# Kernel tuning notes

Hardware: AMD Instinct MI355X
Metric: run time of the kernel (lower is better)

## Reference

```python
import jax, jax.numpy as jnp
import numpy as np

B, S, H, L = 8, 4096, 768, 256   # batch, seq_len, hidden_size, num_lines (= line_ids.max()+1)
ATT_HID = 1024                    # attention MLP hidden dim from nn.Linear(hidden,1024)


def setup_inputs() -> dict:
    key = jax.random.key(0)
    k0, k1, k2, k3 = jax.random.split(key, 4)
    token_hidden = jax.random.normal(k0, (B, S, H), dtype=jnp.float32)
    line_ids = jax.random.randint(k1, (B, S), 0, L)  # all valid; -1 would mark invalid
    W1 = jax.random.normal(k2, (H, ATT_HID), dtype=jnp.float32) * 0.02
    b1 = jnp.zeros((ATT_HID,), jnp.float32)
    W2 = jax.random.normal(k3, (ATT_HID, 1), dtype=jnp.float32) * 0.02
    b2 = jnp.zeros((1,), jnp.float32)
    return {"token_hidden": token_hidden, "line_ids": line_ids,
            "W1": W1, "b1": b1, "W2": W2, "b2": b2}


def reference(token_hidden, line_ids, W1, b1, W2, b2):
    b, s, h = token_hidden.shape
    num_lines = L
    n_seg = b * num_lines + 1  # last segment is a dump slot for invalid (-1) tokens

    # attention scores: Linear -> tanh -> Linear, squeeze(-1)  [b, s]
    scores = (jnp.tanh(token_hidden @ W1 + b1) @ W2 + b2)[..., 0]

    valid = (line_ids >= 0).reshape(-1)                                   # [b*s]
    seg = jnp.where(line_ids >= 0,
                    jnp.arange(b)[:, None] * num_lines + line_ids,
                    b * num_lines).reshape(-1)                            # [b*s]
    s_flat = jnp.where(valid, scores.reshape(-1), -jnp.inf)

    # segment-wise stable softmax
    m = jax.ops.segment_max(s_flat, seg, num_segments=n_seg)
    m = jnp.where(jnp.isfinite(m), m, 0.0)  # empty segments -> safe 0
    e = jnp.where(valid, jnp.exp(scores.reshape(-1) - m[seg]), 0.0)
    denom = jax.ops.segment_sum(e, seg, num_segments=n_seg)
    w = e / jnp.maximum(denom[seg], 1e-20)                                # [b*s]

    # weighted sum of tokens per (batch, line) segment
    feats = jax.ops.segment_sum(token_hidden.reshape(-1, h) * w[:, None],
                                seg, num_segments=n_seg)
    line_features = feats[: b * num_lines].reshape(b, num_lines, h)

    counts = jax.ops.segment_sum(valid.astype(jnp.float32), seg, num_segments=n_seg)
    line_mask = counts[: b * num_lines].reshape(b, num_lines) > 0
    return line_features, line_mask
```

## Files before the change

kernel.cpp:

```cpp
#include <hip/hip_runtime.h>
#include <hip/hip_bf16.h>
#include <string.h>

#define M_TOK 32768
#define H_DIM 768
#define AH    1024
#define NSEG  2048
#define CAP   96
#define CONV_BLOCKS 12288

typedef __attribute__((ext_vector_type(8))) __bf16 bf16x8;
typedef __attribute__((ext_vector_type(4))) float f32x4;

__device__ __forceinline__ float tanh_fast(float x) {
  float e = __expf(2.0f * x);
  return 1.0f - 2.0f * __builtin_amdgcn_rcpf(e + 1.0f);
}

__device__ __forceinline__ float bf2f(unsigned short u) {
  unsigned int v = (unsigned int)u << 16;
  float f;
  memcpy(&f, &v, 4);
  return f;
}

__global__ __launch_bounds__(256) void prep_kernel(
    const float* __restrict__ W1, __hip_bfloat16* __restrict__ W1t,
    const int* __restrict__ line_ids, int* __restrict__ cursor,
    int* __restrict__ order, const float4* __restrict__ X4,
    uint4* __restrict__ Xb4) {
  __shared__ float tile[32][33];
  if (blockIdx.x < 768) {
    int nt = blockIdx.x & 31, ktile = blockIdx.x >> 5;
    int n0 = nt * 32, k0 = ktile * 32;
    int tx = threadIdx.x & 31, ty = threadIdx.x >> 5;
    for (int r = ty; r < 32; r += 8)
      tile[r][tx] = W1[(size_t)(k0 + r) * AH + n0 + tx];
    __syncthreads();
    for (int r = ty; r < 32; r += 8)
      W1t[(size_t)(n0 + r) * H_DIM + k0 + tx] = __float2bfloat16(tile[tx][r]);
  } else if (blockIdx.x < 896) {
    int t = (blockIdx.x - 768) * 256 + threadIdx.x;
    int lid = line_ids[t];
    if (lid >= 0) {
      int seg = (t >> 12) * 256 + lid;
      int pos = atomicAdd(&cursor[seg], 1);
      if (pos < CAP) order[seg * CAP + pos] = t;
    }
  } else {
    int i = (blockIdx.x - 896) * 256 + threadIdx.x;
    float4 v0 = X4[i * 2];
    float4 v1 = X4[i * 2 + 1];
    __hip_bfloat16 h[8] = {
        __float2bfloat16(v0.x), __float2bfloat16(v0.y),
        __float2bfloat16(v0.z), __float2bfloat16(v0.w),
        __float2bfloat16(v1.x), __float2bfloat16(v1.y),
        __float2bfloat16(v1.z), __float2bfloat16(v1.w)};
    uint4 p;
    memcpy(&p, h, 16);
    Xb4[i] = p;
  }
}

__global__ __launch_bounds__(256) void attn_score_kernel(
    const __hip_bfloat16* __restrict__ Xbg,
    const __hip_bfloat16* __restrict__ W1tg, const float* __restrict__ b1g,
    const float* __restrict__ W2g, float* __restrict__ scores) {
  __shared__ __align__(16) __bf16 As[128 * 64];
  __shared__ __align__(16) __bf16 Bs[128 * 64];

  const int tid = threadIdx.x;
  const int bid = blockIdx.x;
  const int xcd = bid & 7;
  const int s   = bid >> 3;
  const int m0  = (xcd * 32 + (s >> 3)) * 128;
  const int n0  = (s & 7) * 128;
  const int lane = tid & 63;
  const int wave = tid >> 6;
  const int wm   = (wave >> 1) * 64;
  const int wn   = (wave & 1) * 64;
  const int ml   = lane & 15;
  const int gsw  = lane & 7;

  const __bf16* Xb = (const __bf16*)Xbg;
  const __bf16* W  = (const __bf16*)W1tg;

  const int srow = tid >> 3;
  const int scol = ((tid & 7) ^ (srow & 7)) * 8;

  f32x4 acc[4][4];
#pragma unroll
  for (int i = 0; i < 4; i++)
#pragma unroll
    for (int j = 0; j < 4; j++) acc[i][j] = (f32x4)0.f;

  for (int kt = 0; kt < H_DIM; kt += 64) {
#pragma unroll
    for (int p = 0; p < 4; ++p) {
      const __bf16* ga = Xb + (size_t)(m0 + p * 32 + srow) * H_DIM + kt + scol;
      __builtin_amdgcn_global_load_lds(
          (const __attribute__((address_space(1))) void*)ga,
          (__attribute__((address_space(3))) void*)&As[p * 2048 + tid * 8],
          16, 0, 0);
      const __bf16* gb = W + (size_t)(n0 + p * 32 + srow) * H_DIM + kt + scol;
      __builtin_amdgcn_global_load_lds(
          (const __attribute__((address_space(1))) void*)gb,
          (__attribute__((address_space(3))) void*)&Bs[p * 2048 + tid * 8],
          16, 0, 0);
    }
    __syncthreads();

#pragma unroll
    for (int c = 0; c < 2; ++c) {
      const int gq = c * 4 + (lane >> 4);
      const int gp = (gq ^ gsw) * 8;
      bf16x8 af[4], bf[4];
#pragma unroll
      for (int i = 0; i < 4; i++)
        af[i] = *(const bf16x8*)&As[(wm + i * 16 + ml) * 64 + gp];
#pragma unroll
      for (int j = 0; j < 4; j++)
        bf[j] = *(const bf16x8*)&Bs[(wn + j * 16 + ml) * 64 + gp];

#pragma unroll
      for (int i = 0; i < 4; i++)
#pragma unroll
        for (int j = 0; j < 4; j++)
          acc[i][j] = __builtin_amdgcn_mfma_f32_16x16x32_bf16(af[i], bf[j],
                                                              acc[i][j], 0, 0, 0);
    }
    __syncthreads();
  }

  float b1v[4], w2v[4];
#pragma unroll
  for (int j = 0; j < 4; j++) {
    int n = n0 + wn + j * 16 + ml;
    b1v[j] = b1g[n];
    w2v[j] = W2g[n];
  }
  const int q4 = (lane >> 4) * 4;
#pragma unroll
  for (int i = 0; i < 4; i++) {
#pragma unroll
    for (int p = 0; p < 4; p++) {
      float t = 0.f;
#pragma unroll
      for (int j = 0; j < 4; j++)
        t += tanh_fast(acc[i][j][p] + b1v[j]) * w2v[j];
      t += __shfl_xor(t, 1);
      t += __shfl_xor(t, 2);
      t += __shfl_xor(t, 4);
      t += __shfl_xor(t, 8);
      if (ml == 0) atomicAdd(&scores[m0 + wm + i * 16 + q4 + p], t);
    }
  }
}

__global__ __launch_bounds__(256) void aggregate_kernel(
    const ushort* __restrict__ Xb, const float* __restrict__ scores,
    const int* __restrict__ cursor, const int* __restrict__ order,
    float4* __restrict__ out4, float* __restrict__ out_mask) {
  __shared__ float sw[CAP];
  __shared__ int   sidx[CAP];
  __shared__ float wred[4];
  const int seg = blockIdx.x;
  const int tid = threadIdx.x;
  int cnt = cursor[seg];
  if (cnt > CAP) cnt = CAP;
  if (tid == 0) out_mask[seg] = cnt > 0 ? 1.f : 0.f;
  if (cnt == 0) {
    if (tid < H_DIM / 4)
      out4[(size_t)seg * (H_DIM / 4) + tid] = make_float4(0.f, 0.f, 0.f, 0.f);
    return;
  }
  const int lane = tid & 63, wave = tid >> 6;
  float lmax = -3.4e38f;
  if (tid < cnt) {
    int idx = order[seg * CAP + tid];
    sidx[tid] = idx;
    float sc = scores[idx];
    sw[tid] = sc;
    lmax = sc;
  }
#pragma unroll
  for (int d = 1; d < 64; d <<= 1) lmax = fmaxf(lmax, __shfl_xor(lmax, d));
  if (lane == 0) wred[wave] = lmax;
  __syncthreads();
  float m = fmaxf(fmaxf(wred[0], wred[1]), fmaxf(wred[2], wred[3]));
  float lsum = 0.f;
  if (tid < cnt) {
    float e = __expf(sw[tid] - m);
    sw[tid] = e;
    lsum = e;
  }
#pragma unroll
  for (int d = 1; d < 64; d <<= 1) lsum += __shfl_xor(lsum, d);
  __syncthreads();
  if (lane == 0) wred[wave] = lsum;
  __syncthreads();
  float denom = wred[0] + wred[1] + wred[2] + wred[3];
  float inv = __builtin_amdgcn_rcpf(fmaxf(denom, 1e-20f));
  if (tid < cnt) sw[tid] *= inv;
  __syncthreads();
  if (tid < H_DIM / 4) {
    const ushort4* base = (const ushort4*)Xb + tid;
    float4 acc = make_float4(0.f, 0.f, 0.f, 0.f);
    int t = 0;
    for (; t + 4 <= cnt; t += 4) {
      ushort4 u0 = base[(size_t)sidx[t]     * (H_DIM / 4)];
      ushort4 u1 = base[(size_t)sidx[t + 1] * (H_DIM / 4)];
      ushort4 u2 = base[(size_t)sidx[t + 2] * (H_DIM / 4)];
      ushort4 u3 = base[(size_t)sidx[t + 3] * (H_DIM / 4)];
      float w0 = sw[t], w1 = sw[t + 1], w2 = sw[t + 2], w3 = sw[t + 3];
      acc.x += w0 * bf2f(u0.x) + w1 * bf2f(u1.x) + w2 * bf2f(u2.x) + w3 * bf2f(u3.x);
      acc.y += w0 * bf2f(u0.y) + w1 * bf2f(u1.y) + w2 * bf2f(u2.y) + w3 * bf2f(u3.y);
      acc.z += w0 * bf2f(u0.z) + w1 * bf2f(u1.z) + w2 * bf2f(u2.z) + w3 * bf2f(u3.z);
      acc.w += w0 * bf2f(u0.w) + w1 * bf2f(u1.w) + w2 * bf2f(u2.w) + w3 * bf2f(u3.w);
    }
    for (; t < cnt; ++t) {
      ushort4 u = base[(size_t)sidx[t] * (H_DIM / 4)];
      float w = sw[t];
      acc.x += w * bf2f(u.x); acc.y += w * bf2f(u.y);
      acc.z += w * bf2f(u.z); acc.w += w * bf2f(u.w);
    }
    out4[(size_t)seg * (H_DIM / 4) + tid] = acc;
  }
}

extern "C" void kernel_launch(void* const* d_in, const int* in_sizes, int n_in,
                              void* d_out, int out_size, void* d_ws, size_t ws_size,
                              hipStream_t stream) {
  const float* X        = (const float*)d_in[0];
  const int*   line_ids = (const int*)d_in[1];
  const float* W1       = (const float*)d_in[2];
  const float* b1       = (const float*)d_in[3];
  const float* W2       = (const float*)d_in[4];

  char* p = (char*)d_ws;
  __hip_bfloat16* Xb  = (__hip_bfloat16*)p;  p += (size_t)M_TOK * H_DIM * 2;
  __hip_bfloat16* W1t = (__hip_bfloat16*)p;  p += 1572864;
  float* scores  = (float*)p;                p += 131072;
  int*   cursor  = (int*)p;                  p += 8192;
  int*   order   = (int*)p;                  p += (size_t)NSEG * CAP * 4;

  float* out_feats = (float*)d_out;
  float* out_mask  = out_feats + (size_t)NSEG * H_DIM;

  hipMemsetAsync(scores, 0, 131072 + 8192, stream);

  prep_kernel<<<896 + CONV_BLOCKS, 256, 0, stream>>>(
      W1, W1t, line_ids, cursor, order, (const float4*)X, (uint4*)Xb);
  attn_score_kernel<<<2048, 256, 0, stream>>>(Xb, W1t, b1, W2, scores);
  aggregate_kernel<<<NSEG, 256, 0, stream>>>((const ushort*)Xb, scores, cursor,
                                             order, (float4*)out_feats, out_mask);
}
```

Baseline: 252.2 us.

## Replace atomics with deterministic partial scores and in-block segment gathering

```diff
diff --git a/kernel.cpp b/kernel.cpp
--- a/kernel.cpp
+++ b/kernel.cpp
@@ -6,7 +6,7 @@
 #define H_DIM 768
 #define AH    1024
 #define NSEG  2048
-#define CAP   96
+#define LCAP  192
 #define CONV_BLOCKS 12288
 
 typedef __attribute__((ext_vector_type(8))) __bf16 bf16x8;
@@ -26,9 +26,7 @@
 
 __global__ __launch_bounds__(256) void prep_kernel(
     const float* __restrict__ W1, __hip_bfloat16* __restrict__ W1t,
-    const int* __restrict__ line_ids, int* __restrict__ cursor,
-    int* __restrict__ order, const float4* __restrict__ X4,
-    uint4* __restrict__ Xb4) {
+    const float4* __restrict__ X4, uint4* __restrict__ Xb4) {
   __shared__ float tile[32][33];
   if (blockIdx.x < 768) {
     int nt = blockIdx.x & 31, ktile = blockIdx.x >> 5;
@@ -39,16 +37,8 @@
     __syncthreads();
     for (int r = ty; r < 32; r += 8)
       W1t[(size_t)(n0 + r) * H_DIM + k0 + tx] = __float2bfloat16(tile[tx][r]);
-  } else if (blockIdx.x < 896) {
-    int t = (blockIdx.x - 768) * 256 + threadIdx.x;
-    int lid = line_ids[t];
-    if (lid >= 0) {
-      int seg = (t >> 12) * 256 + lid;
-      int pos = atomicAdd(&cursor[seg], 1);
-      if (pos < CAP) order[seg * CAP + pos] = t;
-    }
   } else {
-    int i = (blockIdx.x - 896) * 256 + threadIdx.x;
+    int i = (blockIdx.x - 768) * 256 + threadIdx.x;
     float4 v0 = X4[i * 2];
     float4 v1 = X4[i * 2 + 1];
     __hip_bfloat16 h[8] = {
@@ -65,7 +55,7 @@
 __global__ __launch_bounds__(256) void attn_score_kernel(
     const __hip_bfloat16* __restrict__ Xbg,
     const __hip_bfloat16* __restrict__ W1tg, const float* __restrict__ b1g,
-    const float* __restrict__ W2g, float* __restrict__ scores) {
+    const float* __restrict__ W2g, float* __restrict__ scores2) {
   __shared__ __align__(16) __bf16 As[128 * 64];
   __shared__ __align__(16) __bf16 Bs[128 * 64];
 
@@ -74,7 +64,8 @@
   const int xcd = bid & 7;
   const int s   = bid >> 3;
   const int m0  = (xcd * 32 + (s >> 3)) * 128;
-  const int n0  = (s & 7) * 128;
+  const int nt  = s & 7;
+  const int n0  = nt * 128;
   const int lane = tid & 63;
   const int wave = tid >> 6;
   const int wm   = (wave >> 1) * 64;
@@ -140,6 +131,7 @@
     w2v[j] = W2g[n];
   }
   const int q4 = (lane >> 4) * 4;
+  float tval[4][4];
 #pragma unroll
   for (int i = 0; i < 4; i++) {
 #pragma unroll
@@ -152,34 +144,74 @@
       t += __shfl_xor(t, 2);
       t += __shfl_xor(t, 4);
       t += __shfl_xor(t, 8);
-      if (ml == 0) atomicAdd(&scores[m0 + wm + i * 16 + q4 + p], t);
-    }
+      tval[i][p] = t;
+    }
+  }
+  float* redbuf = (float*)As;
+  if ((wave & 1) && ml == 0) {
+#pragma unroll
+    for (int i = 0; i < 4; i++)
+#pragma unroll
+      for (int p = 0; p < 4; p++)
+        redbuf[wm + i * 16 + q4 + p] = tval[i][p];
+  }
+  __syncthreads();
+  if (!(wave & 1) && ml == 0) {
+#pragma unroll
+    for (int i = 0; i < 4; i++)
+#pragma unroll
+      for (int p = 0; p < 4; p++) {
+        int row = wm + i * 16 + q4 + p;
+        scores2[(size_t)(m0 + row) * 8 + nt] = tval[i][p] + redbuf[row];
+      }
   }
 }
 
 __global__ __launch_bounds__(256) void aggregate_kernel(
-    const ushort* __restrict__ Xb, const float* __restrict__ scores,
-    const int* __restrict__ cursor, const int* __restrict__ order,
-    float4* __restrict__ out4, float* __restrict__ out_mask) {
-  __shared__ float sw[CAP];
-  __shared__ int   sidx[CAP];
+    const ushort* __restrict__ Xb, const float* __restrict__ scores2,
+    const int* __restrict__ line_ids, float4* __restrict__ out4,
+    float* __restrict__ out_mask) {
+  __shared__ int   slist[LCAP];
+  __shared__ float sw[LCAP];
+  __shared__ int   wvc[4];
   __shared__ float wred[4];
   const int seg = blockIdx.x;
-  const int tid = threadIdx.x;
-  int cnt = cursor[seg];
-  if (cnt > CAP) cnt = CAP;
+  const int b = seg >> 8, lid = seg & 255;
+  const int tid = threadIdx.x, lane = tid & 63, wave = tid >> 6;
+  const int base = b * 4096;
+
+  int ids[16];
+#pragma unroll
+  for (int c = 0; c < 16; ++c) ids[c] = line_ids[base + c * 256 + tid];
+
+  int total = 0;
+#pragma unroll
+  for (int c = 0; c < 16; ++c) {
+    bool match = (ids[c] == lid);
+    unsigned long long mask = __ballot(match);
+    if (lane == 0) wvc[wave] = __popcll(mask);
+    __syncthreads();
+    int off = total;
+    for (int w = 0; w < wave; ++w) off += wvc[w];
+    if (match) {
+      int pos = off + __popcll(mask & ((1ull << lane) - 1ull));
+      if (pos < LCAP) slist[pos] = base + c * 256 + tid;
+    }
+    total += wvc[0] + wvc[1] + wvc[2] + wvc[3];
+    __syncthreads();
+  }
+  int cnt = total > LCAP ? LCAP : total;
   if (tid == 0) out_mask[seg] = cnt > 0 ? 1.f : 0.f;
   if (cnt == 0) {
     if (tid < H_DIM / 4)
       out4[(size_t)seg * (H_DIM / 4) + tid] = make_float4(0.f, 0.f, 0.f, 0.f);
     return;
   }
-  const int lane = tid & 63, wave = tid >> 6;
   float lmax = -3.4e38f;
   if (tid < cnt) {
-    int idx = order[seg * CAP + tid];
-    sidx[tid] = idx;
-    float sc = scores[idx];
+    const float4* sp = (const float4*)(scores2 + (size_t)slist[tid] * 8);
+    float4 a = sp[0], c4 = sp[1];
+    float sc = ((a.x + a.y) + (a.z + a.w)) + ((c4.x + c4.y) + (c4.z + c4.w));
     sw[tid] = sc;
     lmax = sc;
   }
@@ -204,14 +236,14 @@
   if (tid < cnt) sw[tid] *= inv;
   __syncthreads();
   if (tid < H_DIM / 4) {
-    const ushort4* base = (const ushort4*)Xb + tid;
+    const ushort4* xb = (const ushort4*)Xb + tid;
     float4 acc = make_float4(0.f, 0.f, 0.f, 0.f);
     int t = 0;
     for (; t + 4 <= cnt; t += 4) {
-      ushort4 u0 = base[(size_t)sidx[t]     * (H_DIM / 4)];
-      ushort4 u1 = base[(size_t)sidx[t + 1] * (H_DIM / 4)];
-      ushort4 u2 = base[(size_t)sidx[t + 2] * (H_DIM / 4)];
-      ushort4 u3 = base[(size_t)sidx[t + 3] * (H_DIM / 4)];
+      ushort4 u0 = xb[(size_t)slist[t]     * (H_DIM / 4)];
+      ushort4 u1 = xb[(size_t)slist[t + 1] * (H_DIM / 4)];
+      ushort4 u2 = xb[(size_t)slist[t + 2] * (H_DIM / 4)];
+      ushort4 u3 = xb[(size_t)slist[t + 3] * (H_DIM / 4)];
       float w0 = sw[t], w1 = sw[t + 1], w2 = sw[t + 2], w3 = sw[t + 3];
       acc.x += w0 * bf2f(u0.x) + w1 * bf2f(u1.x) + w2 * bf2f(u2.x) + w3 * bf2f(u3.x);
       acc.y += w0 * bf2f(u0.y) + w1 * bf2f(u1.y) + w2 * bf2f(u2.y) + w3 * bf2f(u3.y);
@@ -219,7 +251,7 @@
       acc.w += w0 * bf2f(u0.w) + w1 * bf2f(u1.w) + w2 * bf2f(u2.w) + w3 * bf2f(u3.w);
     }
     for (; t < cnt; ++t) {
-      ushort4 u = base[(size_t)sidx[t] * (H_DIM / 4)];
+      ushort4 u = xb[(size_t)slist[t] * (H_DIM / 4)];
       float w = sw[t];
       acc.x += w * bf2f(u.x); acc.y += w * bf2f(u.y);
       acc.z += w * bf2f(u.z); acc.w += w * bf2f(u.w);
@@ -238,20 +270,17 @@
   const float* W2       = (const float*)d_in[4];
 
   char* p = (char*)d_ws;
-  __hip_bfloat16* Xb  = (__hip_bfloat16*)p;  p += (size_t)M_TOK * H_DIM * 2;
-  __hip_bfloat16* W1t = (__hip_bfloat16*)p;  p += 1572864;
-  float* scores  = (float*)p;                p += 131072;
-  int*   cursor  = (int*)p;                  p += 8192;
-  int*   order   = (int*)p;                  p += (size_t)NSEG * CAP * 4;
+  __hip_bfloat16* Xb      = (__hip_bfloat16*)p;  p += (size_t)M_TOK * H_DIM * 2;
+  __hip_bfloat16* W1t     = (__hip_bfloat16*)p;  p += 1572864;
+  float*          scores2 = (float*)p;           p += (size_t)M_TOK * 8 * 4;
 
   float* out_feats = (float*)d_out;
   float* out_mask  = out_feats + (size_t)NSEG * H_DIM;
 
-  hipMemsetAsync(scores, 0, 131072 + 8192, stream);
-
-  prep_kernel<<<896 + CONV_BLOCKS, 256, 0, stream>>>(
-      W1, W1t, line_ids, cursor, order, (const float4*)X, (uint4*)Xb);
-  attn_score_kernel<<<2048, 256, 0, stream>>>(Xb, W1t, b1, W2, scores);
-  aggregate_kernel<<<NSEG, 256, 0, stream>>>((const ushort*)Xb, scores, cursor,
-                                             order, (float4*)out_feats, out_mask);
-}
+  prep_kernel<<<768 + CONV_BLOCKS, 256, 0, stream>>>(
+      W1, W1t, (const float4*)X, (uint4*)Xb);
+  attn_score_kernel<<<2048, 256, 0, stream>>>(Xb, W1t, b1, W2, scores2);
+  aggregate_kernel<<<NSEG, 256, 0, stream>>>((const ushort*)Xb, scores2,
+                                             line_ids, (float4*)out_feats,
+                                             out_mask);
+}
```

Measured after the change: 247.7 us, median of 2. Within noise of the previous version (-1.8%).
